# Kernel optimization log

Hardware: AMD Instinct MI355X
Metric: run time of the kernel (lower is better)

## Reference

```python
import jax, jax.numpy as jnp
import numpy as np

B, N, H = 1024, 200, 64


def setup_inputs() -> dict:
    key = jax.random.key(0)
    ks = jax.random.split(key, 8)
    A = jax.random.uniform(ks[0], (B, 2 * N, N), dtype=jnp.float32)
    hidden = jax.random.normal(ks[1], (B, N, H), dtype=jnp.float32)
    s = 1.0 / np.sqrt(H)
    w_ih = jax.random.normal(ks[2], (3 * H, 2 * H), dtype=jnp.float32) * s
    w_hh = jax.random.normal(ks[3], (3 * H, H), dtype=jnp.float32) * s
    b_ih = jnp.zeros((3 * H,), jnp.float32)
    b_hh = jnp.zeros((3 * H,), jnp.float32)
    b_iah = jnp.zeros((H,), jnp.float32)
    b_oah = jnp.zeros((H,), jnp.float32)
    W_in = jax.random.normal(ks[4], (H, H), dtype=jnp.float32) * s
    bias_in = jnp.zeros((H,), jnp.float32)
    W_out = jax.random.normal(ks[5], (H, H), dtype=jnp.float32) * s
    bias_out = jnp.zeros((H,), jnp.float32)
    return {"A": A, "hidden": hidden, "w_ih": w_ih, "w_hh": w_hh,
            "b_ih": b_ih, "b_hh": b_hh, "b_iah": b_iah, "b_oah": b_oah,
            "W_in": W_in, "bias_in": bias_in, "W_out": W_out, "bias_out": bias_out}


def reference(A, hidden, w_ih, w_hh, b_ih, b_hh, b_iah, b_oah,
              W_in, bias_in, W_out, bias_out):
    # SessionGNN._cell, step=1.
    n = A.shape[1] // 2
    A_in, A_out = A[:, :n, :], A[:, n:, :]          # (B, N, N) each
    h_in = jnp.einsum('bnh,gh->bng', hidden, W_in) + bias_in    # (B, N, H)
    h_out = jnp.einsum('bnh,gh->bng', hidden, W_out) + bias_out
    input_in = jnp.matmul(A_in, h_in) + b_iah       # (B, N, H)
    input_out = jnp.matmul(A_out, h_out) + b_oah
    inputs = jnp.concatenate([input_in, input_out], axis=2)     # (B, N, 2H)
    gi = jnp.einsum('bni,gi->bng', inputs, w_ih) + b_ih         # (B, N, 3H)
    gh = jnp.einsum('bnh,gh->bng', hidden, w_hh) + b_hh
    i_r, i_i, i_n = jnp.split(gi, 3, axis=2)
    h_r, h_i, h_n = jnp.split(gh, 3, axis=2)
    resetgate = jax.nn.sigmoid(i_r + h_r)
    inputgate = jax.nn.sigmoid(i_i + h_i)
    newgate = jnp.tanh(i_n + resetgate * h_n)
    return hidden - inputgate * (hidden - newgate)
```

## Files before the change

kernel.cpp:

```cpp
#include <hip/hip_runtime.h>

typedef _Float16 f16;
typedef __attribute__((ext_vector_type(4))) _Float16 f16x4;
typedef __attribute__((ext_vector_type(8))) _Float16 f16x8;
typedef __attribute__((ext_vector_type(4))) float f32x4;

#define MFMA16(a, b, c) __builtin_amdgcn_mfma_f32_16x16x32_f16((a), (b), (c), 0, 0, 0)

__device__ __forceinline__ f16x8 cvt8(float4 a, float4 b) {
    f16x8 r;
    r[0] = (f16)a.x; r[1] = (f16)a.y; r[2] = (f16)a.z; r[3] = (f16)a.w;
    r[4] = (f16)b.x; r[5] = (f16)b.y; r[6] = (f16)b.z; r[7] = (f16)b.w;
    return r;
}

__device__ __forceinline__ f16x8 zero8() {
    f16x8 z;
#pragma unroll
    for (int q = 0; q < 8; ++q) z[q] = (f16)0.0f;
    return z;
}

__global__ void prep_kernel(const float* __restrict__ w_ih, const float* __restrict__ w_hh,
                            const float* __restrict__ b_ih, const float* __restrict__ b_hh,
                            const float* __restrict__ b_iah, const float* __restrict__ b_oah,
                            const float* __restrict__ W_in, const float* __restrict__ bias_in,
                            const float* __restrict__ W_out, const float* __restrict__ bias_out,
                            f16* __restrict__ Wc, f16* __restrict__ Whh, f16* __restrict__ Wih,
                            float* __restrict__ cstA, float* __restrict__ cstB,
                            float* __restrict__ biasc) {
    const int gid = blockIdx.x * 256 + threadIdx.x;
    const int gstride = gridDim.x * 256;
    for (int i = gid; i < 8192; i += gstride)
        Wc[i] = (f16)(i < 4096 ? W_in[i] : W_out[i - 4096]);
    for (int i = gid; i < 12288; i += gstride) Whh[i] = (f16)w_hh[i];
    for (int i = gid; i < 24576; i += gstride) Wih[i] = (f16)w_ih[i];
    for (int job = gid; job < 768; job += gstride) {
        const int g = job >> 2, q = job & 3;
        float s = (q == 0) ? b_ih[g] : 0.0f;
        const float* wr = w_ih + g * 128 + q * 32;
        for (int i = 0; i < 32; ++i)
            s += wr[i] * ((q * 32 + i < 64) ? b_iah[q * 32 + i] : b_oah[q * 32 + i - 64]);
        atomicAdd(&cstA[g], s);
    }
    for (int g = gid; g < 192; g += gstride) cstB[g] = b_hh[g];
    for (int j = gid; j < 128; j += gstride) biasc[j] = (j < 64) ? bias_in[j] : bias_out[j - 64];
}

__global__ void zero_kernel(float* __restrict__ cstA) {
    if (threadIdx.x < 192) cstA[threadIdx.x] = 0.0f;
}

__global__ __launch_bounds__(512, 2) void gru_fused(
    const float* __restrict__ A, const float* __restrict__ hidden,
    const f16* __restrict__ Wc, const f16* __restrict__ Whh, const f16* __restrict__ Wih,
    const float* __restrict__ cstA, const float* __restrict__ cstB,
    const float* __restrict__ biasc, float* __restrict__ out) {
    __shared__ __align__(16) char lds_raw[56576];
    f16* hT  = (f16*)lds_raw;
    f16* hA  = (f16*)lds_raw;
    f16* inp = (f16*)lds_raw;

    const int b = blockIdx.x;
    const float* Ab = A + (size_t)b * 80000;
    const float* hb = hidden + (size_t)b * 12800;
    float* ob = out + (size_t)b * 12800;

    const int tid = threadIdx.x;
    const int w   = tid >> 6;
    const int l   = tid & 63;
    const int l15 = l & 15;
    const int lg  = l >> 4;

    for (int mt = w; mt < 13; mt += 8) {
        const int m  = mt * 16 + l15;
        const int mc = m < 200 ? m : 199;
        const float* hrow = hb + mc * 64;
        float4 r0 = *(const float4*)(hrow + lg * 8);
        float4 r1 = *(const float4*)(hrow + lg * 8 + 4);
        float4 r2 = *(const float4*)(hrow + 32 + lg * 8);
        float4 r3 = *(const float4*)(hrow + 32 + lg * 8 + 4);
        f16x8 a0 = cvt8(r0, r1), a1 = cvt8(r2, r3);
        const int m0 = mt * 16 + lg * 4;
#pragma unroll
        for (int jt = 0; jt < 8; ++jt) {
            const int j = jt * 16 + l15;
            f32x4 acc = {0.f, 0.f, 0.f, 0.f};
            acc = MFMA16(a0, *(const f16x8*)(Wc + j * 64 + lg * 8), acc);
            acc = MFMA16(a1, *(const f16x8*)(Wc + j * 64 + 32 + lg * 8), acc);
            const float bc = biasc[j];
            if (m0 < 200) {
                f16x4 pk;
                pk[0] = (f16)(acc[0] + bc); pk[1] = (f16)(acc[1] + bc);
                pk[2] = (f16)(acc[2] + bc); pk[3] = (f16)(acc[3] + bc);
                *(f16x4*)(hT + j * 200 + m0) = pk;
            }
        }
    }
    __syncthreads();

    f16x8 Bf[7];
    {
        const f16* hTp = hT + (w * 16 + l15) * 200;
#pragma unroll
        for (int ks = 0; ks < 6; ++ks)
            Bf[ks] = *(const f16x8*)(hTp + ks * 32 + lg * 8);
        Bf[6] = (lg == 0) ? *(const f16x8*)(hTp + 192) : zero8();
    }
    __syncthreads();

    const int hf = w >> 2;

    float4 v[7];
#define P2_LOADS(T)                                                               \
    {                                                                             \
        _Pragma("unroll")                                                         \
        for (int r = 0; r < 7; ++r) {                                             \
            const int u = tid + r * 512;                                          \
            if (u < 3200) {                                                       \
                const int uh = u / 1600, rem = u % 1600;                          \
                int grow = (T) * 32 + rem / 50;                                   \
                if (grow > 199) grow = 199;                                       \
                v[r] = *(const float4*)(Ab + (size_t)(uh * 200 + grow) * 200      \
                                        + (rem % 50) * 4);                        \
            }                                                                     \
        }                                                                         \
    }
#define P2_WRITE(BUF)                                                             \
    {                                                                             \
        _Pragma("unroll")                                                         \
        for (int r = 0; r < 7; ++r) {                                             \
            const int u = tid + r * 512;                                          \
            if (u < 3200) {                                                       \
                const int uh = u / 1600, rem = u % 1600;                          \
                f16x4 pk;                                                         \
                pk[0] = (f16)v[r].x; pk[1] = (f16)v[r].y;                         \
                pk[2] = (f16)v[r].z; pk[3] = (f16)v[r].w;                         \
                *(f16x4*)(hA + ((BUF) * 64 + uh * 32 + rem / 50) * 200            \
                          + (rem % 50) * 4) = pk;                                 \
            }                                                                     \
        }                                                                         \
    }

    f32x4 accC[13];
#pragma unroll
    for (int t = 0; t < 13; ++t) accC[t] = (f32x4){0.f, 0.f, 0.f, 0.f};

    P2_LOADS(0);
    P2_WRITE(0);
    P2_LOADS(1);
    __syncthreads();

    for (int t = 0; t < 7; ++t) {
#pragma unroll
        for (int s = 0; s < 2; ++s) {
            if (t == 6 && s == 1) break;
            const f16* hAp = hA + ((t & 1) * 64 + hf * 32 + s * 16 + l15) * 200;
            f32x4 acc = accC[2 * t + s];
#pragma unroll
            for (int ks = 0; ks < 7; ++ks) {
                f16x8 af;
                if (ks < 6)       af = *(const f16x8*)(hAp + ks * 32 + lg * 8);
                else if (lg == 0) af = *(const f16x8*)(hAp + 192);
                else              af = zero8();
                acc = MFMA16(af, Bf[ks], acc);
            }
            accC[2 * t + s] = acc;
        }
        if (t < 6) {
            P2_WRITE((t + 1) & 1);
            if (t < 5) P2_LOADS(t + 2);
        }
        __syncthreads();
    }

#pragma unroll
    for (int u = 0; u < 13; ++u) {
#pragma unroll
        for (int r = 0; r < 4; ++r) {
            const int n = u * 16 + lg * 4 + r;
            if (n < 200) inp[n * 136 + w * 16 + l15] = (f16)accC[u][r];
        }
    }
    __syncthreads();

    const int c    = w & 3;
    const int wm2  = w >> 2;
    const int hcol = c * 16 + l15;
    f16x8 Wf0[4], Wf1[4], Wf2[4];
#pragma unroll
    for (int k = 0; k < 4; ++k) {
        Wf0[k] = *(const f16x8*)(Wih + (hcol      ) * 128 + k * 32 + lg * 8);
        Wf1[k] = *(const f16x8*)(Wih + (64  + hcol) * 128 + k * 32 + lg * 8);
        Wf2[k] = *(const f16x8*)(Wih + (128 + hcol) * 128 + k * 32 + lg * 8);
    }
    f16x8 Hf0[2], Hf1[2], Hf2[2];
#pragma unroll
    for (int k = 0; k < 2; ++k) {
        Hf0[k] = *(const f16x8*)(Whh + (hcol      ) * 64 + k * 32 + lg * 8);
        Hf1[k] = *(const f16x8*)(Whh + (64  + hcol) * 64 + k * 32 + lg * 8);
        Hf2[k] = *(const f16x8*)(Whh + (128 + hcol) * 64 + k * 32 + lg * 8);
    }
    const float cAr = cstA[hcol], cAi = cstA[64 + hcol], cAn = cstA[128 + hcol];
    const float cBr = cstB[hcol], cBi = cstB[64 + hcol], cBn = cstB[128 + hcol];

    for (int t = wm2; t < 13; t += 2) {
        const int n  = t * 16 + l15;
        const int nc = n < 200 ? n : 199;
        f32x4 gir = {0.f,0.f,0.f,0.f}, gii = {0.f,0.f,0.f,0.f}, gin = {0.f,0.f,0.f,0.f};
        f32x4 ghr = {0.f,0.f,0.f,0.f}, ghi = {0.f,0.f,0.f,0.f}, ghn = {0.f,0.f,0.f,0.f};
#pragma unroll
        for (int k = 0; k < 2; ++k) {
            const int h = k * 32 + lg * 8;
            float4 r0 = *(const float4*)(hb + nc * 64 + h);
            float4 r1 = *(const float4*)(hb + nc * 64 + h + 4);
            f16x8 a = cvt8(r0, r1);
            ghr = MFMA16(a, Hf0[k], ghr);
            ghi = MFMA16(a, Hf1[k], ghi);
            ghn = MFMA16(a, Hf2[k], ghn);
        }
#pragma unroll
        for (int k = 0; k < 4; ++k) {
            f16x8 a = *(const f16x8*)(inp + nc * 136 + k * 32 + lg * 8);
            gir = MFMA16(a, Wf0[k], gir);
            gii = MFMA16(a, Wf1[k], gii);
            gin = MFMA16(a, Wf2[k], gin);
        }
#pragma unroll
        for (int r = 0; r < 4; ++r) {
            const int row = t * 16 + lg * 4 + r;
            if (row < 200) {
                const float hv = hb[row * 64 + hcol];
                const float xr = gir[r] + ghr[r] + cAr + cBr;
                const float xi = gii[r] + ghi[r] + cAi + cBi;
                const float rg = 1.0f / (1.0f + __expf(-xr));
                const float ig = 1.0f / (1.0f + __expf(-xi));
                const float xn = gin[r] + cAn + rg * (ghn[r] + cBn);
                const float e2 = __expf(2.0f * xn);
                const float ng = 1.0f - 2.0f / (e2 + 1.0f);
                ob[row * 64 + hcol] = hv + ig * (ng - hv);
            }
        }
    }
}

extern "C" void kernel_launch(void* const* d_in, const int* in_sizes, int n_in,
                              void* d_out, int out_size, void* d_ws, size_t ws_size,
                              hipStream_t stream) {
    const float* A        = (const float*)d_in[0];
    const float* hidden   = (const float*)d_in[1];
    const float* w_ih     = (const float*)d_in[2];
    const float* w_hh     = (const float*)d_in[3];
    const float* b_ih     = (const float*)d_in[4];
    const float* b_hh     = (const float*)d_in[5];
    const float* b_iah    = (const float*)d_in[6];
    const float* b_oah    = (const float*)d_in[7];
    const float* W_in     = (const float*)d_in[8];
    const float* bias_in  = (const float*)d_in[9];
    const float* W_out    = (const float*)d_in[10];
    const float* bias_out = (const float*)d_in[11];
    float* out = (float*)d_out;

    char* wsb = (char*)d_ws;
    f16* Wc      = (f16*)wsb;
    f16* Whh     = Wc + 8192;
    f16* Wih     = Whh + 12288;
    float* cstA  = (float*)(wsb + 90112);
    float* cstB  = cstA + 192;
    float* biasc = cstB + 192;

    zero_kernel<<<dim3(1), dim3(256), 0, stream>>>(cstA);
    prep_kernel<<<dim3(64), dim3(256), 0, stream>>>(
        w_ih, w_hh, b_ih, b_hh, b_iah, b_oah, W_in, bias_in, W_out, bias_out,
        Wc, Whh, Wih, cstA, cstB, biasc);
    gru_fused<<<dim3(1024), dim3(512), 0, stream>>>(
        A, hidden, Wc, Whh, Wih, cstA, cstB, biasc, out);
}
```

Before: 177.1 us.

## Stream adjacency rows from global directly into MFMA fragments, skipping LDS staging

Phase 2 no longer stages A tiles into a double-buffered shared-memory area with block-wide barriers per step. Each wave now loads its own A rows straight from global memory into registers, converts them to fp16 fragments, and prefetches two k-steps ahead. Waves are split by row range (rows 0-6 vs 7-12) and each wave holds two B fragment sets covering 32 output columns. The intermediate inp buffer is written directly per tile with a padded stride of 152. The aim is to remove LDS round trips and the seven synchronisations, at the cost of uncoalesced row-wise global loads, more registers, and larger LDS use that may limit occupancy.

```diff
diff --git a/kernel.cpp b/kernel.cpp
--- a/kernel.cpp
+++ b/kernel.cpp
@@ -56,9 +56,8 @@
     const f16* __restrict__ Wc, const f16* __restrict__ Whh, const f16* __restrict__ Wih,
     const float* __restrict__ cstA, const float* __restrict__ cstB,
     const float* __restrict__ biasc, float* __restrict__ out) {
-    __shared__ __align__(16) char lds_raw[56576];
+    __shared__ __align__(16) char lds_raw[63232];
     f16* hT  = (f16*)lds_raw;
-    f16* hA  = (f16*)lds_raw;
     f16* inp = (f16*)lds_raw;
 
     const int b = blockIdx.x;
@@ -99,89 +98,68 @@
     }
     __syncthreads();
 
-    f16x8 Bf[7];
+    const int g  = w & 3;
+    const int rg = w >> 2;
+    const int hf = g >> 1;
+    f16x8 B0[7], B1[7];
     {
-        const f16* hTp = hT + (w * 16 + l15) * 200;
-#pragma unroll
-        for (int ks = 0; ks < 6; ++ks)
-            Bf[ks] = *(const f16x8*)(hTp + ks * 32 + lg * 8);
-        Bf[6] = (lg == 0) ? *(const f16x8*)(hTp + 192) : zero8();
+        const f16* hT0 = hT + (g * 32 + l15) * 200;
+        const f16* hT1 = hT + (g * 32 + 16 + l15) * 200;
+#pragma unroll
+        for (int ks = 0; ks < 6; ++ks) {
+            B0[ks] = *(const f16x8*)(hT0 + ks * 32 + lg * 8);
+            B1[ks] = *(const f16x8*)(hT1 + ks * 32 + lg * 8);
+        }
+        B0[6] = (lg == 0) ? *(const f16x8*)(hT0 + 192) : zero8();
+        B1[6] = (lg == 0) ? *(const f16x8*)(hT1 + 192) : zero8();
     }
     __syncthreads();
 
-    const int hf = w >> 2;
-
-    float4 v[7];
-#define P2_LOADS(T)                                                               \
+#define AROWP(T) (Ab + (size_t)(hf * 200 + ((((T) * 16 + l15) < 200) ? ((T) * 16 + l15) : 199)) * 200)
+
+    float4 p[2][2];
+
+#define PHASE2(TBEG, NT)                                                          \
     {                                                                             \
+        const float* ap0 = AROWP(TBEG) + lg * 8;                                  \
+        p[0][0] = *(const float4*)ap0;                                            \
+        p[0][1] = *(const float4*)(ap0 + 4);                                      \
+        const float* ap1 = AROWP(TBEG) + 32 + lg * 8;                             \
+        p[1][0] = *(const float4*)ap1;                                            \
+        p[1][1] = *(const float4*)(ap1 + 4);                                      \
         _Pragma("unroll")                                                         \
-        for (int r = 0; r < 7; ++r) {                                             \
-            const int u = tid + r * 512;                                          \
-            if (u < 3200) {                                                       \
-                const int uh = u / 1600, rem = u % 1600;                          \
-                int grow = (T) * 32 + rem / 50;                                   \
-                if (grow > 199) grow = 199;                                       \
-                v[r] = *(const float4*)(Ab + (size_t)(uh * 200 + grow) * 200      \
-                                        + (rem % 50) * 4);                        \
+        for (int tt = 0; tt < (NT); ++tt) {                                       \
+            const int t = (TBEG) + tt;                                            \
+            f32x4 a0 = {0.f, 0.f, 0.f, 0.f}, a1 = {0.f, 0.f, 0.f, 0.f};           \
+            _Pragma("unroll")                                                     \
+            for (int k = 0; k < 7; ++k) {                                         \
+                const int s = tt * 7 + k;                                         \
+                float4 q0 = p[s & 1][0], q1 = p[s & 1][1];                        \
+                const int ns = s + 2, nt = ns / 7, nk = ns % 7;                   \
+                if (nt < (NT)) {                                                  \
+                    const float* ap = AROWP((TBEG) + nt)                          \
+                                      + (nk < 6 ? nk * 32 + lg * 8 : 192);        \
+                    p[s & 1][0] = *(const float4*)ap;                             \
+                    p[s & 1][1] = *(const float4*)(ap + 4);                       \
+                }                                                                 \
+                f16x8 af = (k == 6 && lg != 0) ? zero8() : cvt8(q0, q1);          \
+                a0 = MFMA16(af, B0[k], a0);                                       \
+                a1 = MFMA16(af, B1[k], a1);                                       \
+            }                                                                     \
+            _Pragma("unroll")                                                     \
+            for (int r = 0; r < 4; ++r) {                                         \
+                const int n = t * 16 + lg * 4 + r;                                \
+                if (n < 200) {                                                    \
+                    inp[n * 152 + g * 32 + l15]      = (f16)a0[r];                \
+                    inp[n * 152 + g * 32 + 16 + l15] = (f16)a1[r];                \
+                }                                                                 \
             }                                                                     \
         }                                                                         \
     }
-#define P2_WRITE(BUF)                                                             \
-    {                                                                             \
-        _Pragma("unroll")                                                         \
-        for (int r = 0; r < 7; ++r) {                                             \
-            const int u = tid + r * 512;                                          \
-            if (u < 3200) {                                                       \
-                const int uh = u / 1600, rem = u % 1600;                          \
-                f16x4 pk;                                                         \
-                pk[0] = (f16)v[r].x; pk[1] = (f16)v[r].y;                         \
-                pk[2] = (f16)v[r].z; pk[3] = (f16)v[r].w;                         \
-                *(f16x4*)(hA + ((BUF) * 64 + uh * 32 + rem / 50) * 200            \
-                          + (rem % 50) * 4) = pk;                                 \
-            }                                                                     \
-        }                                                                         \
-    }
-
-    f32x4 accC[13];
-#pragma unroll
-    for (int t = 0; t < 13; ++t) accC[t] = (f32x4){0.f, 0.f, 0.f, 0.f};
-
-    P2_LOADS(0);
-    P2_WRITE(0);
-    P2_LOADS(1);
-    __syncthreads();
-
-    for (int t = 0; t < 7; ++t) {
-#pragma unroll
-        for (int s = 0; s < 2; ++s) {
-            if (t == 6 && s == 1) break;
-            const f16* hAp = hA + ((t & 1) * 64 + hf * 32 + s * 16 + l15) * 200;
-            f32x4 acc = accC[2 * t + s];
-#pragma unroll
-            for (int ks = 0; ks < 7; ++ks) {
-                f16x8 af;
-                if (ks < 6)       af = *(const f16x8*)(hAp + ks * 32 + lg * 8);
-                else if (lg == 0) af = *(const f16x8*)(hAp + 192);
-                else              af = zero8();
-                acc = MFMA16(af, Bf[ks], acc);
-            }
-            accC[2 * t + s] = acc;
-        }
-        if (t < 6) {
-            P2_WRITE((t + 1) & 1);
-            if (t < 5) P2_LOADS(t + 2);
-        }
-        __syncthreads();
-    }
-
-#pragma unroll
-    for (int u = 0; u < 13; ++u) {
-#pragma unroll
-        for (int r = 0; r < 4; ++r) {
-            const int n = u * 16 + lg * 4 + r;
-            if (n < 200) inp[n * 136 + w * 16 + l15] = (f16)accC[u][r];
-        }
-    }
+
+    if (rg == 0) PHASE2(0, 7) else PHASE2(7, 6)
+#undef PHASE2
+#undef AROWP
     __syncthreads();
 
     const int c    = w & 3;
@@ -221,7 +199,7 @@
         }
 #pragma unroll
         for (int k = 0; k < 4; ++k) {
-            f16x8 a = *(const f16x8*)(inp + nc * 136 + k * 32 + lg * 8);
+            f16x8 a = *(const f16x8*)(inp + nc * 152 + k * 32 + lg * 8);
             gir = MFMA16(a, Wf0[k], gir);
             gii = MFMA16(a, Wf1[k], gii);
             gin = MFMA16(a, Wf2[k], gin);
@@ -233,9 +211,9 @@
                 const float hv = hb[row * 64 + hcol];
                 const float xr = gir[r] + ghr[r] + cAr + cBr;
                 const float xi = gii[r] + ghi[r] + cAi + cBi;
-                const float rg = 1.0f / (1.0f + __expf(-xr));
+                const float rg2 = 1.0f / (1.0f + __expf(-xr));
                 const float ig = 1.0f / (1.0f + __expf(-xi));
-                const float xn = gin[r] + cAn + rg * (ghn[r] + cBn);
+                const float xn = gin[r] + cAn + rg2 * (ghn[r] + cBn);
                 const float e2 = __expf(2.0f * xn);
                 const float ng = 1.0f - 2.0f / (e2 + 1.0f);
                 ob[row * 64 + hcol] = hv + ig * (ng - hv);
```

New measurement: 169.3 us. 4.4% less time.

## Stream adjacency tiles directly into LDS with global_load_lds and convert on read

Applied to the files above, without the earlier changes.

Replaces the register-staged load/convert/store of adjacency rows with direct global-to-LDS 16-byte transfers, keeping fp32 in LDS and converting to fp16 when fragments are read for MFMA. The tile is shrunk to 16 rows per stage with 13 double-buffered steps, and the next stage's transfer is issued before the current compute. The aim is to free the registers used for staging and overlap global loads with MFMA work. In exchange, LDS reads double because the data is fp32, conversions move into the inner loop, and the loop now has more barriers.

```diff
diff --git a/kernel.cpp b/kernel.cpp
--- a/kernel.cpp
+++ b/kernel.cpp
@@ -6,6 +6,11 @@
 typedef __attribute__((ext_vector_type(4))) float f32x4;
 
 #define MFMA16(a, b, c) __builtin_amdgcn_mfma_f32_16x16x32_f16((a), (b), (c), 0, 0, 0)
+
+#define GLOAD_LDS16(GP, LP)                                                       \
+    __builtin_amdgcn_global_load_lds(                                             \
+        (const __attribute__((address_space(1))) unsigned int*)(GP),              \
+        (__attribute__((address_space(3))) unsigned int*)(LP), 16, 0, 0)
 
 __device__ __forceinline__ f16x8 cvt8(float4 a, float4 b) {
     f16x8 r;
@@ -56,10 +61,10 @@
     const f16* __restrict__ Wc, const f16* __restrict__ Whh, const f16* __restrict__ Wih,
     const float* __restrict__ cstA, const float* __restrict__ cstB,
     const float* __restrict__ biasc, float* __restrict__ out) {
-    __shared__ __align__(16) char lds_raw[56576];
-    f16* hT  = (f16*)lds_raw;
-    f16* hA  = (f16*)lds_raw;
-    f16* inp = (f16*)lds_raw;
+    __shared__ __align__(16) char lds_raw[54400];
+    f16* hT    = (f16*)lds_raw;
+    float* hAf = (float*)lds_raw;
+    f16* inp   = (f16*)lds_raw;
 
     const int b = blockIdx.x;
     const float* Ab = A + (size_t)b * 80000;
@@ -111,81 +116,71 @@
 
     const int hf = w >> 2;
 
-    float4 v[7];
-#define P2_LOADS(T)                                                               \
+#define P2_STAGE(T, BUF)                                                          \
     {                                                                             \
         _Pragma("unroll")                                                         \
-        for (int r = 0; r < 7; ++r) {                                             \
-            const int u = tid + r * 512;                                          \
-            if (u < 3200) {                                                       \
-                const int uh = u / 1600, rem = u % 1600;                          \
-                int grow = (T) * 32 + rem / 50;                                   \
+        for (int r = 0; r < 4; ++r) {                                             \
+            const int u0 = w * 64 + r * 512;                                      \
+            if (u0 < 1600) {                                                      \
+                const int u = u0 + l;                                             \
+                const int uh = u / 800, rem = u % 800;                            \
+                int grow = (T) * 16 + rem / 50;                                   \
                 if (grow > 199) grow = 199;                                       \
-                v[r] = *(const float4*)(Ab + (size_t)(uh * 200 + grow) * 200      \
-                                        + (rem % 50) * 4);                        \
+                const float* gsrc = Ab + (size_t)(uh * 200 + grow) * 200          \
+                                    + (rem % 50) * 4;                             \
+                float* ldst = hAf + (size_t)(BUF) * 6400 + (size_t)u0 * 4;        \
+                GLOAD_LDS16(gsrc, ldst);                                          \
             }                                                                     \
         }                                                                         \
     }
-#define P2_WRITE(BUF)                                                             \
-    {                                                                             \
-        _Pragma("unroll")                                                         \
-        for (int r = 0; r < 7; ++r) {                                             \
-            const int u = tid + r * 512;                                          \
-            if (u < 3200) {                                                       \
-                const int uh = u / 1600, rem = u % 1600;                          \
-                f16x4 pk;                                                         \
-                pk[0] = (f16)v[r].x; pk[1] = (f16)v[r].y;                         \
-                pk[2] = (f16)v[r].z; pk[3] = (f16)v[r].w;                         \
-                *(f16x4*)(hA + ((BUF) * 64 + uh * 32 + rem / 50) * 200            \
-                          + (rem % 50) * 4) = pk;                                 \
-            }                                                                     \
-        }                                                                         \
-    }
 
     f32x4 accC[13];
 #pragma unroll
     for (int t = 0; t < 13; ++t) accC[t] = (f32x4){0.f, 0.f, 0.f, 0.f};
 
-    P2_LOADS(0);
-    P2_WRITE(0);
-    P2_LOADS(1);
-    __syncthreads();
-
-    for (int t = 0; t < 7; ++t) {
-#pragma unroll
-        for (int s = 0; s < 2; ++s) {
-            if (t == 6 && s == 1) break;
-            const f16* hAp = hA + ((t & 1) * 64 + hf * 32 + s * 16 + l15) * 200;
-            f32x4 acc = accC[2 * t + s];
+    P2_STAGE(0, 0);
+    __syncthreads();
+
+#pragma unroll
+    for (int t = 0; t < 13; ++t) {
+        if (t < 12) P2_STAGE(t + 1, (t + 1) & 1);
+        {
+            const float* hAp = hAf + (t & 1) * 6400 + hf * 3200 + l15 * 200;
+            f32x4 acc = accC[t];
 #pragma unroll
             for (int ks = 0; ks < 7; ++ks) {
                 f16x8 af;
-                if (ks < 6)       af = *(const f16x8*)(hAp + ks * 32 + lg * 8);
-                else if (lg == 0) af = *(const f16x8*)(hAp + 192);
-                else              af = zero8();
+                if (ks < 6) {
+                    float4 q0 = *(const float4*)(hAp + ks * 32 + lg * 8);
+                    float4 q1 = *(const float4*)(hAp + ks * 32 + lg * 8 + 4);
+                    af = cvt8(q0, q1);
+                } else if (lg == 0) {
+                    float4 q0 = *(const float4*)(hAp + 192);
+                    float4 q1 = *(const float4*)(hAp + 196);
+                    af = cvt8(q0, q1);
+                } else {
+                    af = zero8();
+                }
                 acc = MFMA16(af, Bf[ks], acc);
             }
-            accC[2 * t + s] = acc;
-        }
-        if (t < 6) {
-            P2_WRITE((t + 1) & 1);
-            if (t < 5) P2_LOADS(t + 2);
+            accC[t] = acc;
         }
         __syncthreads();
     }
-
-#pragma unroll
-    for (int u = 0; u < 13; ++u) {
+#undef P2_STAGE
+
+#pragma unroll
+    for (int t = 0; t < 13; ++t) {
 #pragma unroll
         for (int r = 0; r < 4; ++r) {
-            const int n = u * 16 + lg * 4 + r;
-            if (n < 200) inp[n * 136 + w * 16 + l15] = (f16)accC[u][r];
-        }
-    }
-    __syncthreads();
-
-    const int c    = w & 3;
-    const int wm2  = w >> 2;
+            const int n = t * 16 + lg * 4 + r;
+            if (n < 200) inp[n * 136 + w * 16 + l15] = (f16)accC[t][r];
+        }
+    }
+    __syncthreads();
+
+    const int c   = w & 3;
+    const int wm2 = w >> 2;
     const int hcol = c * 16 + l15;
     f16x8 Wf0[4], Wf1[4], Wf2[4];
 #pragma unroll
```

After: 213.4 us. +20.5%, slower.
